# Kernel tuning notes

Measured on AMD Instinct MI355X. Metric: run time of the kernel, lower is better.

## Reference

```python
import jax, jax.numpy as jnp
import numpy as np

N = 65536      # batch of CPU-state samples
D = 64         # byte-embedding dim
H = 512        # expert hidden dim
V = 256        # byte vocabulary / result logits
NFLAGS = 8
# number of embedded inputs per expert
KS = {"alu": 4, "logic": 4, "move": 5, "flow": 6, "stack": 6}


def setup_inputs() -> dict:
    key = jax.random.key(0)
    ks = list(jax.random.split(key, 64))
    nk = lambda: ks.pop()
    rint = lambda mx: jax.random.randint(nk(), (N,), 0, mx, dtype=jnp.int32)
    inp = {n: rint(256) for n in ["A", "X", "Y", "SP", "P", "PCH", "PCL", "Op", "Val"]}
    # deterministic opcode -> functional-unit map (stand-in for build_fu_map)
    inp["fu_map"] = (jnp.arange(256, dtype=jnp.int32) % 5)
    p = lambda shape: jax.random.normal(nk(), shape, dtype=jnp.float32) * 0.02
    for name, k in KS.items():
        inp[f"{name}_emb"] = p((k, V, D))
        inp[f"{name}_W1"] = p((k * D, H))
        inp[f"{name}_b1"] = jnp.zeros((H,), jnp.float32)
    inp["alu_Wr"] = p((H, V)); inp["alu_Wf"] = p((H, NFLAGS))
    inp["logic_Wr"] = p((H, V)); inp["logic_Wf"] = p((H, NFLAGS))
    inp["move_Wo"] = p((H, V))
    inp["flow_Wo"] = p((H, V))
    inp["stack_Wo"] = p((H, V))
    return inp


def _expert_hidden(emb, idx_list, W1, b1):
    # emb: [k, 256, D]; idx_list: k arrays of [N] byte indices
    ids = jnp.stack(idx_list)                                  # [k, N]
    f = emb[jnp.arange(emb.shape[0])[:, None], ids]            # [k, N, D] gather
    f = jnp.moveaxis(f, 0, 1).reshape(ids.shape[1], -1)        # [N, k*D]
    return jax.nn.gelu(f @ W1 + b1)                            # [N, H]


def reference(A, X, Y, SP, P, PCH, PCL, Op, Val, fu_map,
              alu_emb, alu_W1, alu_b1, alu_Wr, alu_Wf,
              logic_emb, logic_W1, logic_b1, logic_Wr, logic_Wf,
              move_emb, move_W1, move_b1, move_Wo,
              flow_emb, flow_W1, flow_b1, flow_Wo,
              stack_emb, stack_W1, stack_b1, stack_Wo):
    # deterministic zero-cost router: opcode -> FU id
    fu = fu_map[Op]                                            # [N]
    carry = P & 1                                              # carry bit of status reg
    mask = lambda k: (fu == k)[:, None].astype(jnp.float32)
    # ALU (FU 0): a, operand, carry, opcode -> result + flags logits
    h = _expert_hidden(alu_emb, [A, Val, carry, Op], alu_W1, alu_b1)
    alu = jnp.concatenate([h @ alu_Wr, h @ alu_Wf], -1) * mask(0)      # [N, 264]
    # LOGIC (FU 1): same inputs, separate params
    h = _expert_hidden(logic_emb, [A, Val, carry, Op], logic_W1, logic_b1)
    logic = jnp.concatenate([h @ logic_Wr, h @ logic_Wf], -1) * mask(1)  # [N, 264]
    # MOVE (FU 2): a, x, y, operand, opcode
    move = (_expert_hidden(move_emb, [A, X, Y, Val, Op], move_W1, move_b1) @ move_Wo) * mask(2)
    # FLOW (FU 3): pc (as PCH,PCL bytes), flags, target, sp, opcode
    flow = (_expert_hidden(flow_emb, [PCH, PCL, P, Val, SP, Op], flow_W1, flow_b1) @ flow_Wo) * mask(3)
    # STACK (FU 4): a, x, sp, flags, stack_top, opcode
    stack = (_expert_hidden(stack_emb, [A, X, SP, P, Val, Op], stack_W1, stack_b1) @ stack_Wo) * mask(4)
    # dense capacity-1 dispatch: each sample's row is nonzero only in its FU's slice
    return jnp.concatenate([alu, logic, move, flow, stack], -1)        # [N, 1296]
```

## Files before the change

kernel.cpp:

```cpp
#include <hip/hip_runtime.h>

#define DEV __device__ __forceinline__

typedef __attribute__((ext_vector_type(8))) short short8;
typedef __attribute__((ext_vector_type(4))) float f32x4;
typedef unsigned short u16;

struct Ptrs { const void* p[32]; };

constexpr int N_TOK = 65536;
constexpr int cK  [5] = {4,4,5,6,6};
constexpr int cK1 [5] = {256,256,320,384,384};
constexpr int cN2 [5] = {264,264,256,256,256};
constexpr int cNT [5] = {17,17,16,16,16};
constexpr int cC0 [5] = {0,264,528,784,1040};
constexpr int cKID[5][6] = {{0,8,9,7,0,0},{0,8,9,7,0,0},{0,1,2,8,7,0},
                            {5,6,4,8,3,7},{0,1,3,4,8,7}};
constexpr int cEOFF[5] = {0,65536,131072,212992,311296};
constexpr int cWOFF[5] = {0,131072,262144,425984,622592};
constexpr int cHOFF[5] = {0,139264,278528,417792,557056};
constexpr int EMB_TOT = 409600, W1_TOT = 819200, HEAD_TOT = 696320;
constexpr int PREP_TOT = EMB_TOT + W1_TOT + HEAD_TOT;

constexpr size_t WS_COUNTS = 0;
constexpr size_t WS_BUCKET = 256;
constexpr size_t WS_EMB    = 256 + (size_t)5 * N_TOK * 4;
constexpr size_t WS_W1T    = WS_EMB + (size_t)EMB_TOT * 2;
constexpr size_t WS_HT     = WS_W1T + (size_t)W1_TOT * 2;
constexpr size_t WS_COMP   = WS_HT + (size_t)HEAD_TOT * 2;
constexpr int    COMP_STRIDE = 272;

constexpr int ROWS = 128;
constexpr int HP   = 520;

constexpr int TOK_OFF = 0;
constexpr int IDS_OFF = 512;
constexpr int BUF_OFF = 3584;
constexpr int LDS_BYTES = BUF_OFF + 135168;

DEV u16 f2bf(float f) {
  unsigned u = __builtin_bit_cast(unsigned, f);
  u += 0x7FFFu + ((u >> 16) & 1u);
  return (u16)(u >> 16);
}

DEV float gelu_f(float x) {
  float u = 0.7978845608028654f * x * (1.0f + 0.044715f * x * x);
  float t2 = fminf(fmaxf(2.0f * u, -30.0f), 30.0f);
  float e = __expf(t2);
  float th = (e - 1.0f) / (e + 1.0f);
  return 0.5f * x * (1.0f + th);
}

__global__ __launch_bounds__(256) void prep_kernel(Ptrs in, u16* embB, u16* w1tB, u16* hTB) {
  int idx = blockIdx.x * 256 + threadIdx.x;
  if (idx < EMB_TOT) {
    int e = 0, off = idx;
    while (off >= cK[e] * 16384) { off -= cK[e] * 16384; ++e; }
    const float* src = (const float*)in.p[10 + 3*e];
    embB[cEOFF[e] + off] = f2bf(src[off]);
  } else if (idx < EMB_TOT + W1_TOT) {
    int off = idx - EMB_TOT;
    int e = 0;
    while (off >= 512 * cK1[e]) { off -= 512 * cK1[e]; ++e; }
    int K1 = cK1[e];
    int n = off / K1, k = off - n * K1;
    const float* w1 = (const float*)in.p[11 + 3*e];
    w1tB[cWOFF[e] + off] = f2bf(w1[k * 512 + n]);
  } else {
    int off = idx - (EMB_TOT + W1_TOT);
    int e = off / 139264, r = off - e * 139264;
    int n = r >> 9, k = r & 511;
    float v = 0.0f;
    if (e < 2) {
      if (n < 256)       v = ((const float*)in.p[25 + 2*e])[k * 256 + n];
      else if (n < 264)  v = ((const float*)in.p[26 + 2*e])[k * 8 + (n - 256)];
    } else {
      if (n < 256)       v = ((const float*)in.p[29 + (e - 2)])[k * 256 + n];
    }
    hTB[cHOFF[e] + r] = f2bf(v);
  }
}

__global__ __launch_bounds__(256) void bucket_kernel(const int* Op, const int* fu_map,
                                                     int* counts, int* buckets) {
  __shared__ int lc[5], lb[5];
  int tid = threadIdx.x;
  if (tid < 5) lc[tid] = 0;
  __syncthreads();
  int t = blockIdx.x * 256 + tid;
  int fu = fu_map[Op[t]];
  int lp = atomicAdd(&lc[fu], 1);
  __syncthreads();
  if (tid < 5) lb[tid] = atomicAdd(&counts[tid], lc[tid]);
  __syncthreads();
  buckets[fu * N_TOK + lb[fu] + lp] = t;
}

template<int E>
DEV void expert_tile(const Ptrs& in, int tile, int count, const int* buckets,
                     const u16* embB, const u16* w1tB, const u16* hTB,
                     float* comp, char* smem) {
  constexpr int K1 = cK1[E], KT = cK1[E] / 32, N2 = cN2[E];
  constexpr int NT = cNT[E], KE = cK[E];
  constexpr int FB  = K1 * 2;
  constexpr int CPR = KE * 8;

  u16*   hbuf = (u16*)(smem + BUF_OFF);
  float* rbuf = (float*)(smem + BUF_OFF);
  int*   tokb = (int*)(smem + TOK_OFF);
  int*   idsb = (int*)(smem + IDS_OFF);

  const int tid = threadIdx.x;
  const int vr = min(count - tile * ROWS, ROWS);
  const int rbase = E * N_TOK + tile * ROWS;

  __syncthreads();

  if (tid < ROWS)
    tokb[tid] = (tid < vr) ? buckets[rbase + tid] : -1;
  for (int i = tid; i < ROWS * KE; i += 512) {
    int r = i / KE, k = i - r * KE;
    int t = buckets[rbase + ((r < vr) ? r : 0)];
    int s = cKID[E][k];
    int v = (s == 9) ? (((const int*)in.p[4])[t] & 1)
                     : ((const int*)in.p[s])[t];
    idsb[r * 6 + k] = v;
  }
  __syncthreads();

  const int lane = tid & 63, wave = tid >> 6;
  const int l15 = lane & 15, lq = (lane >> 4) & 3;

  {
    const u16* embE = embB + cEOFF[E];
    short8 val[KT];
    int    dst[KT];
    #pragma unroll
    for (int it = 0; it < KT; ++it) {
      int d = tid + it * 512;
      int r = d / CPR, c = d - r * CPR;
      int k = c >> 3;
      int id = idsb[r * 6 + k];
      val[it] = *(const short8*)(embE + (size_t)((k * 256 + id) << 6) + ((c & 7) << 3));
      dst[it] = BUF_OFF + r * FB + ((c * 16) ^ ((r & 7) << 4));
    }
    #pragma unroll
    for (int it = 0; it < KT; ++it)
      *(short8*)(smem + dst[it]) = val[it];
  }
  __syncthreads();

  const u16* w1e  = w1tB + cWOFF[E];
  const float* b1 = (const float*)in.p[12 + 3 * E];

  f32x4 acc[8][4];
  {
    const f32x4 z = {0.f, 0.f, 0.f, 0.f};
    #pragma unroll
    for (int m = 0; m < 8; ++m)
      #pragma unroll
      for (int nt = 0; nt < 4; ++nt) acc[m][nt] = z;
  }
  #pragma unroll 2
  for (int kt = 0; kt < KT; ++kt) {
    short8 a[8], b[4];
    #pragma unroll
    for (int m = 0; m < 8; ++m) {
      int row = m * 16 + l15;
      a[m] = *(const short8*)(smem + BUF_OFF + row * FB +
                              ((kt * 64 + lq * 16) ^ ((row & 7) << 4)));
    }
    #pragma unroll
    for (int nt = 0; nt < 4; ++nt)
      b[nt] = *(const short8*)(w1e + (wave * 64 + nt * 16 + l15) * K1 + kt * 32 + lq * 8);
    #pragma unroll
    for (int nt = 0; nt < 4; ++nt)
      #pragma unroll
      for (int m = 0; m < 8; ++m)
        acc[m][nt] = __builtin_amdgcn_mfma_f32_16x16x32_bf16(a[m], b[nt], acc[m][nt], 0, 0, 0);
  }
  __syncthreads();

  #pragma unroll
  for (int nt = 0; nt < 4; ++nt) {
    int col = wave * 64 + nt * 16 + l15;
    float b1v = b1[col];
    #pragma unroll
    for (int m = 0; m < 8; ++m)
      #pragma unroll
      for (int q = 0; q < 4; ++q)
        hbuf[(m * 16 + lq * 4 + q) * HP + col] = f2bf(gelu_f(acc[m][nt][q] + b1v));
  }
  __syncthreads();

  const u16* hTe = hTB + cHOFF[E];
  f32x4 acc2[8][3];
  {
    const f32x4 z = {0.f, 0.f, 0.f, 0.f};
    #pragma unroll
    for (int m = 0; m < 8; ++m)
      #pragma unroll
      for (int j = 0; j < 3; ++j) acc2[m][j] = z;
  }
  #pragma unroll 4
  for (int kt = 0; kt < 16; ++kt) {
    short8 a[8];
    #pragma unroll
    for (int m = 0; m < 8; ++m)
      a[m] = *(const short8*)(hbuf + (m * 16 + l15) * HP + kt * 32 + lq * 8);
    #pragma unroll
    for (int j = 0; j < 3; ++j) {
      int nt = wave + 8 * j;
      if (nt >= NT) break;
      short8 b = *(const short8*)(hTe + (nt * 16 + l15) * 512 + kt * 32 + lq * 8);
      #pragma unroll
      for (int m = 0; m < 8; ++m)
        acc2[m][j] = __builtin_amdgcn_mfma_f32_16x16x32_bf16(a[m], b, acc2[m][j], 0, 0, 0);
    }
  }
  __syncthreads();

  #pragma unroll
  for (int j = 0; j < 3; ++j) {
    int nt = wave + 8 * j;
    if (nt >= NT) break;
    int coln = nt * 16 + l15;
    if (coln < N2) {
      #pragma unroll
      for (int m = 0; m < 8; ++m)
        #pragma unroll
        for (int q = 0; q < 4; ++q)
          rbuf[(m * 16 + lq * 4 + q) * N2 + coln] = acc2[m][j][q];
    }
  }
  __syncthreads();

  {
    constexpr int V = N2 / 4;
    int tot = vr * V;
    for (int idx = tid; idx < tot; idx += 512) {
      int r = idx / V, c = idx - r * V;
      int t = tokb[r];
      f32x4 v = *(const f32x4*)(rbuf + r * N2 + c * 4);
      __builtin_nontemporal_store(v, (f32x4*)(comp + (size_t)t * COMP_STRIDE + c * 4));
    }
  }
}

__global__ __launch_bounds__(512, 1) void moe_kernel(Ptrs in, const int* counts,
                                                     const int* buckets,
                                                     const u16* embB, const u16* w1tB,
                                                     const u16* hTB, float* comp) {
  extern __shared__ char smem[];
  int c0 = counts[0], c1 = counts[1], c2 = counts[2], c3 = counts[3], c4 = counts[4];
  int t0 = (c0 + ROWS - 1) / ROWS;
  int t1 = (c1 + ROWS - 1) / ROWS;
  int t2 = (c2 + ROWS - 1) / ROWS;
  int t3 = (c3 + ROWS - 1) / ROWS;
  int t4 = (c4 + ROWS - 1) / ROWS;
  int p1 = t0, p2 = p1 + t1, p3 = p2 + t2, p4 = p3 + t3, p5 = p4 + t4;

  const int x = blockIdx.x & 7;
  const int slot = blockIdx.x >> 3;
  const int beg = (x * p5) >> 3;
  const int end = ((x + 1) * p5) >> 3;

  for (int g = beg + slot; g < end; g += 64) {
    int e = 0, base = 0, cnt = c0;
    if (g >= p1) { e = 1; base = p1; cnt = c1; }
    if (g >= p2) { e = 2; base = p2; cnt = c2; }
    if (g >= p3) { e = 3; base = p3; cnt = c3; }
    if (g >= p4) { e = 4; base = p4; cnt = c4; }
    int tile = g - base;
    switch (e) {
      case 0: expert_tile<0>(in, tile, cnt, buckets, embB, w1tB, hTB, comp, smem); break;
      case 1: expert_tile<1>(in, tile, cnt, buckets, embB, w1tB, hTB, comp, smem); break;
      case 2: expert_tile<2>(in, tile, cnt, buckets, embB, w1tB, hTB, comp, smem); break;
      case 3: expert_tile<3>(in, tile, cnt, buckets, embB, w1tB, hTB, comp, smem); break;
      case 4: expert_tile<4>(in, tile, cnt, buckets, embB, w1tB, hTB, comp, smem); break;
    }
  }
}

__global__ __launch_bounds__(256) void expand_kernel(const int* Op, const int* fu_map,
                                                     const float* comp, float* out) {
  const int lane = threadIdx.x & 63, wv = threadIdx.x >> 6;
  for (int t = blockIdx.x * 4 + wv; t < N_TOK; t += gridDim.x * 4) {
    int fu = fu_map[Op[t]];
    int c0q = cC0[fu] >> 2;
    int n2q = cN2[fu] >> 2;
    const float* cr = comp + (size_t)t * COMP_STRIDE;
    float* orow = out + (size_t)t * 1296;
    #pragma unroll
    for (int it = 0; it < 6; ++it) {
      int c4 = it * 64 + lane;
      if (c4 < 324) {
        f32x4 v = {0.f, 0.f, 0.f, 0.f};
        int rel = c4 - c0q;
        if (rel >= 0 && rel < n2q) v = *(const f32x4*)(cr + rel * 4);
        __builtin_nontemporal_store(v, (f32x4*)(orow + c4 * 4));
      }
    }
  }
}

extern "C" void kernel_launch(void* const* d_in, const int* in_sizes, int n_in,
                              void* d_out, int out_size, void* d_ws, size_t ws_size,
                              hipStream_t stream) {
  char* ws = (char*)d_ws;
  int* counts  = (int*)(ws + WS_COUNTS);
  int* buckets = (int*)(ws + WS_BUCKET);
  u16* embB    = (u16*)(ws + WS_EMB);
  u16* w1tB    = (u16*)(ws + WS_W1T);
  u16* hTB     = (u16*)(ws + WS_HT);
  float* comp  = (float*)(ws + WS_COMP);

  Ptrs P;
  for (int i = 0; i < 32; ++i) P.p[i] = d_in[i];

  (void)hipMemsetAsync(counts, 0, 5 * sizeof(int), stream);
  prep_kernel<<<PREP_TOT / 256, 256, 0, stream>>>(P, embB, w1tB, hTB);
  bucket_kernel<<<N_TOK / 256, 256, 0, stream>>>((const int*)d_in[7], (const int*)d_in[9],
                                                 counts, buckets);
  moe_kernel<<<512, 512, LDS_BYTES, stream>>>(P, counts, buckets, embB, w1tB, hTB, comp);
  expand_kernel<<<2048, 256, 0, stream>>>((const int*)d_in[7], (const int*)d_in[9],
                                          comp, (float*)d_out);
}
```

Measured before the change: 273.1 us.

## Store expert results in bucket order, prefetch weights, halve MoE grid

Expert tiles now write their results contiguously in bucket order instead of scattering rows by token id. The bucket kernel records each token's position so the expand kernel can gather from the compact buffer. Both GEMM loops software-prefetch the next k-step of weight fragments into registers, and the MoE grid drops from 512 to 256 blocks with the loop stride adjusted to match. The contiguous stores should coalesce better, at the cost of an extra position array and a scattered read in expand. Prefetching raises register pressure, and fewer blocks may lower occupancy or leave CUs idle.

After: 249.3 us. 8.7% less time.

```diff
diff --git a/kernel.cpp b/kernel.cpp
--- a/kernel.cpp
+++ b/kernel.cpp
@@ -27,8 +27,9 @@
 constexpr size_t WS_EMB    = 256 + (size_t)5 * N_TOK * 4;
 constexpr size_t WS_W1T    = WS_EMB + (size_t)EMB_TOT * 2;
 constexpr size_t WS_HT     = WS_W1T + (size_t)W1_TOT * 2;
-constexpr size_t WS_COMP   = WS_HT + (size_t)HEAD_TOT * 2;
-constexpr int    COMP_STRIDE = 272;
+constexpr size_t WS_POS    = WS_HT + (size_t)HEAD_TOT * 2;
+constexpr size_t WS_COMP   = WS_POS + (size_t)N_TOK * 4;
+constexpr int    RP = 272;
 
 constexpr int ROWS = 128;
 constexpr int HP   = 520;
@@ -36,7 +37,8 @@
 constexpr int TOK_OFF = 0;
 constexpr int IDS_OFF = 512;
 constexpr int BUF_OFF = 3584;
-constexpr int LDS_BYTES = BUF_OFF + 135168;
+constexpr int BUF_SZ  = ROWS * RP * 4;
+constexpr int LDS_BYTES = BUF_OFF + BUF_SZ;
 
 DEV u16 f2bf(float f) {
   unsigned u = __builtin_bit_cast(unsigned, f);
@@ -83,7 +85,7 @@
 }
 
 __global__ __launch_bounds__(256) void bucket_kernel(const int* Op, const int* fu_map,
-                                                     int* counts, int* buckets) {
+                                                     int* counts, int* buckets, int* posOf) {
   __shared__ int lc[5], lb[5];
   int tid = threadIdx.x;
   if (tid < 5) lc[tid] = 0;
@@ -94,11 +96,13 @@
   __syncthreads();
   if (tid < 5) lb[tid] = atomicAdd(&counts[tid], lc[tid]);
   __syncthreads();
-  buckets[fu * N_TOK + lb[fu] + lp] = t;
+  int pos = lb[fu] + lp;
+  buckets[fu * N_TOK + pos] = t;
+  posOf[t] = pos;
 }
 
 template<int E>
-DEV void expert_tile(const Ptrs& in, int tile, int count, const int* buckets,
+DEV void expert_tile(const Ptrs& in, int tile, int count, int gbase, const int* buckets,
                      const u16* embB, const u16* w1tB, const u16* hTB,
                      float* comp, char* smem) {
   constexpr int K1 = cK1[E], KT = cK1[E] / 32, N2 = cN2[E];
@@ -129,9 +133,6 @@
   }
   __syncthreads();
 
-  const int lane = tid & 63, wave = tid >> 6;
-  const int l15 = lane & 15, lq = (lane >> 4) & 3;
-
   {
     const u16* embE = embB + cEOFF[E];
     short8 val[KT];
@@ -151,6 +152,9 @@
   }
   __syncthreads();
 
+  const int lane = tid & 63, wave = tid >> 6;
+  const int l15 = lane & 15, lq = (lane >> 4) & 3;
+
   const u16* w1e  = w1tB + cWOFF[E];
   const float* b1 = (const float*)in.p[12 + 3 * E];
 
@@ -162,23 +166,32 @@
       #pragma unroll
       for (int nt = 0; nt < 4; ++nt) acc[m][nt] = z;
   }
-  #pragma unroll 2
-  for (int kt = 0; kt < KT; ++kt) {
-    short8 a[8], b[4];
-    #pragma unroll
-    for (int m = 0; m < 8; ++m) {
-      int row = m * 16 + l15;
-      a[m] = *(const short8*)(smem + BUF_OFF + row * FB +
-                              ((kt * 64 + lq * 16) ^ ((row & 7) << 4)));
-    }
+  {
+    short8 bcur[4], bnxt[4];
     #pragma unroll
     for (int nt = 0; nt < 4; ++nt)
-      b[nt] = *(const short8*)(w1e + (wave * 64 + nt * 16 + l15) * K1 + kt * 32 + lq * 8);
-    #pragma unroll
-    for (int nt = 0; nt < 4; ++nt)
-      #pragma unroll
-      for (int m = 0; m < 8; ++m)
-        acc[m][nt] = __builtin_amdgcn_mfma_f32_16x16x32_bf16(a[m], b[nt], acc[m][nt], 0, 0, 0);
+      bcur[nt] = *(const short8*)(w1e + (wave * 64 + nt * 16 + l15) * K1 + lq * 8);
+    #pragma unroll 2
+    for (int kt = 0; kt < KT; ++kt) {
+      if (kt + 1 < KT) {
+        #pragma unroll
+        for (int nt = 0; nt < 4; ++nt)
+          bnxt[nt] = *(const short8*)(w1e + (wave * 64 + nt * 16 + l15) * K1 + (kt + 1) * 32 + lq * 8);
+      }
+      #pragma unroll
+      for (int m = 0; m < 8; ++m) {
+        int r = m * 16 + l15;
+        short8 a = *(const short8*)(smem + BUF_OFF + r * FB +
+                                    (((kt * 4 + lq) << 4) ^ ((r & 7) << 4)));
+        #pragma unroll
+        for (int nt = 0; nt < 4; ++nt)
+          acc[m][nt] = __builtin_amdgcn_mfma_f32_16x16x32_bf16(a, bcur[nt], acc[m][nt], 0, 0, 0);
+      }
+      if (kt + 1 < KT) {
+        #pragma unroll
+        for (int nt = 0; nt < 4; ++nt) bcur[nt] = bnxt[nt];
+      }
+    }
   }
   __syncthreads();
 
@@ -203,20 +216,38 @@
       #pragma unroll
       for (int j = 0; j < 3; ++j) acc2[m][j] = z;
   }
-  #pragma unroll 4
-  for (int kt = 0; kt < 16; ++kt) {
-    short8 a[8];
-    #pragma unroll
-    for (int m = 0; m < 8; ++m)
-      a[m] = *(const short8*)(hbuf + (m * 16 + l15) * HP + kt * 32 + lq * 8);
+  {
+    short8 b2cur[3], b2nxt[3];
     #pragma unroll
     for (int j = 0; j < 3; ++j) {
       int nt = wave + 8 * j;
-      if (nt >= NT) break;
-      short8 b = *(const short8*)(hTe + (nt * 16 + l15) * 512 + kt * 32 + lq * 8);
-      #pragma unroll
-      for (int m = 0; m < 8; ++m)
-        acc2[m][j] = __builtin_amdgcn_mfma_f32_16x16x32_bf16(a[m], b, acc2[m][j], 0, 0, 0);
+      if (nt < NT)
+        b2cur[j] = *(const short8*)(hTe + (nt * 16 + l15) * 512 + lq * 8);
+    }
+    #pragma unroll 2
+    for (int kt = 0; kt < 16; ++kt) {
+      if (kt < 15) {
+        #pragma unroll
+        for (int j = 0; j < 3; ++j) {
+          int nt = wave + 8 * j;
+          if (nt < NT)
+            b2nxt[j] = *(const short8*)(hTe + (nt * 16 + l15) * 512 + (kt + 1) * 32 + lq * 8);
+        }
+      }
+      #pragma unroll
+      for (int m = 0; m < 8; ++m) {
+        short8 a = *(const short8*)(hbuf + (m * 16 + l15) * HP + kt * 32 + lq * 8);
+        #pragma unroll
+        for (int j = 0; j < 3; ++j) {
+          int nt = wave + 8 * j;
+          if (nt < NT)
+            acc2[m][j] = __builtin_amdgcn_mfma_f32_16x16x32_bf16(a, b2cur[j], acc2[m][j], 0, 0, 0);
+        }
+      }
+      if (kt < 15) {
+        #pragma unroll
+        for (int j = 0; j < 3; ++j) b2cur[j] = b2nxt[j];
+      }
     }
   }
   __syncthreads();
@@ -224,27 +255,24 @@
   #pragma unroll
   for (int j = 0; j < 3; ++j) {
     int nt = wave + 8 * j;
-    if (nt >= NT) break;
-    int coln = nt * 16 + l15;
-    if (coln < N2) {
-      #pragma unroll
-      for (int m = 0; m < 8; ++m)
-        #pragma unroll
-        for (int q = 0; q < 4; ++q)
-          rbuf[(m * 16 + lq * 4 + q) * N2 + coln] = acc2[m][j][q];
-    }
-  }
-  __syncthreads();
-
-  {
-    constexpr int V = N2 / 4;
-    int tot = vr * V;
-    for (int idx = tid; idx < tot; idx += 512) {
-      int r = idx / V, c = idx - r * V;
-      int t = tokb[r];
-      f32x4 v = *(const f32x4*)(rbuf + r * N2 + c * 4);
-      __builtin_nontemporal_store(v, (f32x4*)(comp + (size_t)t * COMP_STRIDE + c * 4));
-    }
+    if (nt < NT) {
+      int coln = nt * 16 + l15;
+      if (coln < N2) {
+        #pragma unroll
+        for (int m = 0; m < 8; ++m)
+          #pragma unroll
+          for (int q = 0; q < 4; ++q)
+            rbuf[(m * 16 + lq * 4 + q) * RP + coln] = acc2[m][j][q];
+      }
+    }
+  }
+  __syncthreads();
+
+  {
+    float* dstc = comp + (size_t)(gbase + tile * ROWS) * RP;
+    const int tot = vr * (RP / 4);
+    for (int idx = tid; idx < tot; idx += 512)
+      *(f32x4*)(dstc + idx * 4) = *(const f32x4*)(rbuf + idx * 4);
   }
 }
 
@@ -260,37 +288,43 @@
   int t3 = (c3 + ROWS - 1) / ROWS;
   int t4 = (c4 + ROWS - 1) / ROWS;
   int p1 = t0, p2 = p1 + t1, p3 = p2 + t2, p4 = p3 + t3, p5 = p4 + t4;
+  int b1 = c0, b2 = b1 + c1, b3 = b2 + c2, b4 = b3 + c3;
 
   const int x = blockIdx.x & 7;
   const int slot = blockIdx.x >> 3;
   const int beg = (x * p5) >> 3;
   const int end = ((x + 1) * p5) >> 3;
 
-  for (int g = beg + slot; g < end; g += 64) {
-    int e = 0, base = 0, cnt = c0;
-    if (g >= p1) { e = 1; base = p1; cnt = c1; }
-    if (g >= p2) { e = 2; base = p2; cnt = c2; }
-    if (g >= p3) { e = 3; base = p3; cnt = c3; }
-    if (g >= p4) { e = 4; base = p4; cnt = c4; }
+  for (int g = beg + slot; g < end; g += 32) {
+    int e = 0, base = 0, cnt = c0, gb = 0;
+    if (g >= p1) { e = 1; base = p1; cnt = c1; gb = b1; }
+    if (g >= p2) { e = 2; base = p2; cnt = c2; gb = b2; }
+    if (g >= p3) { e = 3; base = p3; cnt = c3; gb = b3; }
+    if (g >= p4) { e = 4; base = p4; cnt = c4; gb = b4; }
     int tile = g - base;
     switch (e) {
-      case 0: expert_tile<0>(in, tile, cnt, buckets, embB, w1tB, hTB, comp, smem); break;
-      case 1: expert_tile<1>(in, tile, cnt, buckets, embB, w1tB, hTB, comp, smem); break;
-      case 2: expert_tile<2>(in, tile, cnt, buckets, embB, w1tB, hTB, comp, smem); break;
-      case 3: expert_tile<3>(in, tile, cnt, buckets, embB, w1tB, hTB, comp, smem); break;
-      case 4: expert_tile<4>(in, tile, cnt, buckets, embB, w1tB, hTB, comp, smem); break;
+      case 0: expert_tile<0>(in, tile, cnt, gb, buckets, embB, w1tB, hTB, comp, smem); break;
+      case 1: expert_tile<1>(in, tile, cnt, gb, buckets, embB, w1tB, hTB, comp, smem); break;
+      case 2: expert_tile<2>(in, tile, cnt, gb, buckets, embB, w1tB, hTB, comp, smem); break;
+      case 3: expert_tile<3>(in, tile, cnt, gb, buckets, embB, w1tB, hTB, comp, smem); break;
+      case 4: expert_tile<4>(in, tile, cnt, gb, buckets, embB, w1tB, hTB, comp, smem); break;
     }
   }
 }
 
 __global__ __launch_bounds__(256) void expand_kernel(const int* Op, const int* fu_map,
+                                                     const int* counts, const int* posOf,
                                                      const float* comp, float* out) {
+  int b[5];
+  b[0] = 0; b[1] = counts[0]; b[2] = b[1] + counts[1];
+  b[3] = b[2] + counts[2]; b[4] = b[3] + counts[3];
   const int lane = threadIdx.x & 63, wv = threadIdx.x >> 6;
   for (int t = blockIdx.x * 4 + wv; t < N_TOK; t += gridDim.x * 4) {
     int fu = fu_map[Op[t]];
+    int slot = b[fu] + posOf[t];
     int c0q = cC0[fu] >> 2;
     int n2q = cN2[fu] >> 2;
-    const float* cr = comp + (size_t)t * COMP_STRIDE;
+    const float* cr = comp + (size_t)slot * RP;
     float* orow = out + (size_t)t * 1296;
     #pragma unroll
     for (int it = 0; it < 6; ++it) {
@@ -314,6 +348,7 @@
   u16* embB    = (u16*)(ws + WS_EMB);
   u16* w1tB    = (u16*)(ws + WS_W1T);
   u16* hTB     = (u16*)(ws + WS_HT);
+  int* posOf   = (int*)(ws + WS_POS);
   float* comp  = (float*)(ws + WS_COMP);
 
   Ptrs P;
@@ -322,8 +357,8 @@
   (void)hipMemsetAsync(counts, 0, 5 * sizeof(int), stream);
   prep_kernel<<<PREP_TOT / 256, 256, 0, stream>>>(P, embB, w1tB, hTB);
   bucket_kernel<<<N_TOK / 256, 256, 0, stream>>>((const int*)d_in[7], (const int*)d_in[9],
-                                                 counts, buckets);
-  moe_kernel<<<512, 512, LDS_BYTES, stream>>>(P, counts, buckets, embB, w1tB, hTB, comp);
+                                                 counts, buckets, posOf);
+  moe_kernel<<<256, 512, LDS_BYTES, stream>>>(P, counts, buckets, embB, w1tB, hTB, comp);
   expand_kernel<<<2048, 256, 0, stream>>>((const int*)d_in[7], (const int*)d_in[9],
-                                          comp, (float*)d_out);
-}
+                                          counts, posOf, comp, (float*)d_out);
+}
```
